# Kernel optimization log

Measured on AMD Instinct MI355X. Metric: run time of the kernel, lower is better.

## Reference

```python
import jax, jax.numpy as jnp
import numpy as np

N_BLOCKS = 16
N_HEADS = 2
HEAD_DIM = 32
SCALE = HEAD_DIM ** (-0.5)


def setup_inputs() -> dict:
    key = jax.random.key(0)
    ks = jax.random.split(key, 5)
    b, s, d = 16, 4096, 1024
    nb, bd = N_BLOCKS, 1024 // N_BLOCKS  # block_dim = 64; emb per-block dim = 64
    w_std = 1.0 / np.sqrt(bd)
    inp = {
        'x': jax.random.normal(ks[0], (b, s, d), dtype=jnp.float32),
        'wq': jax.random.normal(ks[1], (nb, bd, bd), dtype=jnp.float32) * w_std,
        'bq': jnp.zeros((nb, bd), dtype=jnp.float32),
        'wk': jax.random.normal(ks[2], (nb, bd, bd), dtype=jnp.float32) * w_std,
        'bk': jnp.zeros((nb, bd), dtype=jnp.float32),
        'wv': jax.random.normal(ks[3], (nb, bd, bd), dtype=jnp.float32) * w_std,
        'bv': jnp.zeros((nb, bd), dtype=jnp.float32),
        'wf': jax.random.normal(ks[4], (nb, bd, bd), dtype=jnp.float32) * w_std,
        'bf': jnp.zeros((nb, bd), dtype=jnp.float32),
    }
    return inp


def _group_linear(x, w, b):
    # x: [B, S, G*I] -> per-block linear -> [B, S, G*O]
    B, S, _ = x.shape
    G, I, O = w.shape
    xg = x.reshape(B, S, G, I)
    y = jnp.einsum('bsgi,gio->bsgo', xg, w) + b
    return y.reshape(B, S, G * O)


def reference(x, wq, bq, wk, bk, wv, bv, wf, bf):
    B, S, D = x.shape
    nb, nh, hd = N_BLOCKS, N_HEADS, HEAD_DIM
    # grouped QKV projections -> [B, S, nb, nh, hd] -> heads before blocks
    q = _group_linear(x, wq, bq).reshape(B, S, nb, nh, hd).transpose(0, 1, 3, 2, 4) * SCALE
    k = _group_linear(x, wk, bk).reshape(B, S, nb, nh, hd).transpose(0, 1, 3, 2, 4)
    v = _group_linear(x, wv, bv).reshape(B, S, nb, nh, hd).transpose(0, 1, 3, 2, 4)
    # attention across blocks: score [B, S, nh, nb, nb]
    score = jnp.einsum('bshgd,bshfd->bshgf', q, k)
    score = jax.nn.softmax(score, axis=-1)
    out = jnp.einsum('bshgf,bshfd->bshgd', score, v)
    # back to [B, S, nb, nh, hd] then flatten
    out = out.transpose(0, 1, 3, 2, 4).reshape(B, S, nb * nh * hd)
    out = _group_linear(out, wf, bf)
    return out.reshape(B, S, D)
```

## Files before the change

### kernel.cpp

```cpp
#include <hip/hip_runtime.h>
#include <hip/hip_bf16.h>
#include <stdint.h>


typedef __attribute__((ext_vector_type(8))) short bf16x8;
typedef __attribute__((ext_vector_type(4))) float f32x4;

#define NTOK   65536
#define DM     1024
#define TT     16
#define QSCALE 0.17677669529663687f
#define LOG2E  1.4426950408889634f

static __device__ __forceinline__ unsigned short f2bf(float f) {
  unsigned int u = __float_as_uint(f);
  u += 0x7fffu + ((u >> 16) & 1u);
  return (unsigned short)(u >> 16);
}

static __device__ __forceinline__ unsigned int pk2(float a, float b) {
  return (unsigned int)f2bf(a) | ((unsigned int)f2bf(b) << 16);
}

static __device__ __forceinline__ bf16x8 pack8(float4 a, float4 b) {
  bf16x8 r;
  r[0] = (short)f2bf(a.x); r[1] = (short)f2bf(a.y);
  r[2] = (short)f2bf(a.z); r[3] = (short)f2bf(a.w);
  r[4] = (short)f2bf(b.x); r[5] = (short)f2bf(b.y);
  r[6] = (short)f2bf(b.z); r[7] = (short)f2bf(b.w);
  return r;
}

union FragCast { uint4 u4; bf16x8 v; uint2 u2[2]; unsigned int u[4]; };

__global__ void build_wfrag(const float* __restrict__ wq, const float* __restrict__ wk,
                            const float* __restrict__ wv, const float* __restrict__ wf,
                            uint4* __restrict__ wfrag) {
  int tid = blockIdx.x * 256 + threadIdx.x;
  if (tid >= 4 * 16 * 2 * 4 * 64) return;
  int lane =  tid        & 63;
  int nf   = (tid >> 6)  & 3;
  int kk   = (tid >> 8)  & 1;
  int g    = (tid >> 9)  & 15;
  int mat  =  tid >> 13;
  const float* w = (mat == 0) ? wq : (mat == 1) ? wk : (mat == 2) ? wv : wf;
  float sc = (mat == 0) ? QSCALE : 1.0f;
  int o  = nf * 16 + (lane & 15);
  int kb = kk * 32 + 8 * (lane >> 4);
  unsigned int packed[4];
#pragma unroll
  for (int jj = 0; jj < 4; ++jj) {
    unsigned short lo = f2bf(w[(g * 64 + kb + 2 * jj    ) * 64 + o] * sc);
    unsigned short hi = f2bf(w[(g * 64 + kb + 2 * jj + 1) * 64 + o] * sc);
    packed[jj] = (unsigned int)lo | ((unsigned int)hi << 16);
  }
  uint4 u; u.x = packed[0]; u.y = packed[1]; u.z = packed[2]; u.w = packed[3];
  wfrag[tid] = u;
}

#define PH1(h_) do {                                                          \
  _Pragma("unroll")                                                           \
  for (int gi = 0; gi < 2; ++gi) {                                            \
    const int g = 2 * w + gi;                                                 \
    _Pragma("unroll")                                                         \
    for (int mat = 0; mat < 2; ++mat) {       \
      const float* bp = mat ? bk : bq;                                        \
      const float bsc = mat ? 1.0f : QSCALE;                                  \
      unsigned short* dst = mat ? s_k : s_q;                                  \
      _Pragma("unroll")                                                       \
      for (int nf2 = 0; nf2 < 2; ++nf2) {                                     \
        const int nf = 2 * (h_) + nf2;                                        \
        float4 b4 = *(const float4*)&bp[g * 64 + nf * 16 + 4 * lq];           \
        f32x4 a1 = {b4.x * bsc, b4.y * bsc, b4.z * bsc, b4.w * bsc};          \
        _Pragma("unroll")                                                     \
        for (int kk = 0; kk < 2; ++kk) {                                      \
          FragCast fc;                                                        \
          fc.u4 = wfrag[(((mat * 16 + g) * 2 + kk) * 4 + nf) * 64 + lane];    \
          a1 = __builtin_amdgcn_mfma_f32_16x16x32_bf16(fc.v, afr[gi][kk], a1, 0, 0, 0); \
        }                                                                     \
             \
        uint2 w2; w2.x = pk2(a1[0], a1[1]); w2.y = pk2(a1[2], a1[3]);         \
        const int blk = (16 * (2 * nf2 + (lq >> 1)) + g) ^ (lr & 7);          \
        *(uint2*)&dst[lr * 512 + blk * 8 + 4 * (lq & 1)] = w2;                \
      }                                                                       \
    }                                                                         \
    _Pragma("unroll")                                                         \
    for (int nf2 = 0; nf2 < 2; ++nf2) {         \
      const int nf = 2 * (h_) + nf2;                                          \
      const float bias = bv[g * 64 + nf * 16 + lr];                           \
      f32x4 a1 = {bias, bias, bias, bias};                                    \
      _Pragma("unroll")                                                       \
      for (int kk = 0; kk < 2; ++kk) {                                        \
        FragCast fc;                                                          \
        fc.u4 = wfrag[(((2 * 16 + g) * 2 + kk) * 4 + nf) * 64 + lane];        \
        a1 = __builtin_amdgcn_mfma_f32_16x16x32_bf16(afr[gi][kk], fc.v, a1, 0, 0, 0); \
      }                                                                       \
                   \
      const int L = 16 * (g >> 2) + lr;                                       \
      const int jj = g & 3;                                                   \
      _Pragma("unroll")                                                       \
      for (int r = 0; r < 4; ++r)                                             \
        s_v[((4 * lq + r) * 2 + nf2) * 256 + L * 4 + jj] = f2bf(a1[r]);       \
    }                                                                         \
  }                                                                           \
} while (0)

#define PH2() do {                                                            \
  _Pragma("unroll")                                                           \
  for (int tt = 0; tt < 2; ++tt) {                                            \
    const int t = 2 * w + tt;                                                 \
    f32x4 zero = {0.f, 0.f, 0.f, 0.f};                                        \
    FragCast qa, ka;                                                          \
    const int blk = lane ^ (t & 7);                                           \
    qa.u4 = *(const uint4*)&s_q[t * 512 + blk * 8];                           \
    ka.u4 = *(const uint4*)&s_k[t * 512 + blk * 8];                           \
                  \
    f32x4 sc4 = __builtin_amdgcn_mfma_f32_16x16x32_bf16(ka.v, qa.v, zero, 0, 0, 0); \
    float m = fmaxf(fmaxf(sc4[0], sc4[1]), fmaxf(sc4[2], sc4[3]));            \
    m = fmaxf(m, __shfl_xor(m, 16));                                          \
    m = fmaxf(m, __shfl_xor(m, 32));                                          \
    float p0 = exp2f((sc4[0] - m) * LOG2E);                                   \
    float p1 = exp2f((sc4[1] - m) * LOG2E);                                   \
    float p2 = exp2f((sc4[2] - m) * LOG2E);                                   \
    float p3 = exp2f((sc4[3] - m) * LOG2E);                                   \
    float s = p0 + p1 + p2 + p3;                                              \
    s += __shfl_xor(s, 16);                                                   \
    s += __shfl_xor(s, 32);                                                   \
    const float inv = __fdividef(1.0f, s);                                    \
    FragCast pa;                      \
    pa.u[0] = pk2(p0 * inv, p1 * inv);                                        \
    pa.u[1] = pk2(p2 * inv, p3 * inv);                                        \
    pa.u[2] = 0; pa.u[3] = 0;                                                 \
    _Pragma("unroll")                                                         \
    for (int nf = 0; nf < 2; ++nf) {                                          \
      FragCast va;              \
      va.u2[0] = *(const uint2*)&s_v[(t * 2 + nf) * 256 + lane * 4];          \
      va.u[2] = 0; va.u[3] = 0;                                               \
      f32x4 o4 = __builtin_amdgcn_mfma_f32_16x16x32_bf16(va.v, pa.v, zero, 0, 0, 0); \
                                   \
      uint2 w2; w2.x = pk2(o4[0], o4[1]); w2.y = pk2(o4[2], o4[3]);           \
      const int ablk = (16 * (2 * nf + (lq >> 1)) + lr) ^ (t & 7);            \
      *(uint2*)&s_att[t * 512 + ablk * 8 + 4 * (lq & 1)] = w2;                \
    }                                                                         \
  }                                                                           \
} while (0)

#define PH3(h_) do {                                                          \
  _Pragma("unroll")                                                           \
  for (int gi = 0; gi < 2; ++gi) {                                            \
    const int g = 2 * w + gi;                                                 \
    FragCast aa;                        \
    const int blk = (16 * lq + g) ^ (lr & 7);                                 \
    aa.u4 = *(const uint4*)&s_att[lr * 512 + blk * 8];                        \
    _Pragma("unroll")                                                         \
    for (int nf = 0; nf < 4; ++nf) {                                          \
      FragCast fc;                                                            \
      fc.u4 = wfrag[(((3 * 16 + g) * 2 + (h_)) * 4 + nf) * 64 + lane];        \
      acc[gi][nf] = __builtin_amdgcn_mfma_f32_16x16x32_bf16(fc.v, aa.v, acc[gi][nf], 0, 0, 0); \
    }                                                                         \
  }                                                                           \
} while (0)

__global__ __launch_bounds__(512, 4)
void fused_gc(const float* __restrict__ x,
              const float* __restrict__ bq, const float* __restrict__ bk,
              const float* __restrict__ bv, const float* __restrict__ bfb,
              const uint4* __restrict__ wfrag,
              float* __restrict__ out) {
  __shared__ __align__(16) unsigned short s_q  [16 * 512];
  __shared__ __align__(16) unsigned short s_k  [16 * 512];
  __shared__ __align__(16) unsigned short s_att[16 * 512];
  __shared__ __align__(16) unsigned short s_v  [16 * 2 * 64 * 4];

  const int tid  = threadIdx.x;
  const int w    = tid >> 6;
  const int lane = tid & 63;
  const int lr   = lane & 15;
  const int lq   = lane >> 4;
  const long tok0 = (long)blockIdx.x * TT;

  bf16x8 afr[2][2];
  {
    const float* xr = x + (tok0 + lr) * DM;
#pragma unroll
    for (int gi = 0; gi < 2; ++gi) {
      const int g = 2 * w + gi;
#pragma unroll
      for (int kk = 0; kk < 2; ++kk) {
        const float* p = xr + g * 64 + kk * 32 + 8 * lq;
        afr[gi][kk] = pack8(*(const float4*)p, *(const float4*)(p + 4));
      }
    }
  }

  f32x4 acc[2][4];

  PH1(0);
  __syncthreads();
  PH2();
  __syncthreads();

#pragma unroll
  for (int gi = 0; gi < 2; ++gi) {
    const int g = 2 * w + gi;
#pragma unroll
    for (int nf = 0; nf < 4; ++nf) {
      float4 b4 = *(const float4*)&bfb[g * 64 + nf * 16 + 4 * lq];
      acc[gi][nf][0] = b4.x; acc[gi][nf][1] = b4.y;
      acc[gi][nf][2] = b4.z; acc[gi][nf][3] = b4.w;
    }
  }
  PH3(0);
  PH1(1);
  __syncthreads();
  PH2();
  __syncthreads();
  PH3(1);

#pragma unroll
  for (int gi = 0; gi < 2; ++gi) {
    const int g = 2 * w + gi;
#pragma unroll
    for (int nf = 0; nf < 4; ++nf) {
      float4 o4;
      o4.x = acc[gi][nf][0]; o4.y = acc[gi][nf][1];
      o4.z = acc[gi][nf][2]; o4.w = acc[gi][nf][3];
      *(float4*)&out[(tok0 + lr) * DM + g * 64 + nf * 16 + 4 * lq] = o4;
    }
  }
}

extern "C" void kernel_launch(void* const* d_in, const int* in_sizes, int n_in,
                              void* d_out, int out_size, void* d_ws, size_t ws_size,
                              hipStream_t stream) {
  const float* x   = (const float*)d_in[0];
  const float* wq  = (const float*)d_in[1];
  const float* bq_ = (const float*)d_in[2];
  const float* wk  = (const float*)d_in[3];
  const float* bk_ = (const float*)d_in[4];
  const float* wv  = (const float*)d_in[5];
  const float* bv_ = (const float*)d_in[6];
  const float* wf  = (const float*)d_in[7];
  const float* bf_ = (const float*)d_in[8];
  (void)in_sizes; (void)n_in; (void)out_size; (void)ws_size;

  uint4* wfrag = (uint4*)d_ws;

  build_wfrag<<<128, 256, 0, stream>>>(wq, wk, wv, wf, wfrag);
  fused_gc<<<NTOK / TT, 512, 0, stream>>>(x, bq_, bk_, bv_, bf_, wfrag,
                                          (float*)d_out);
}
```

Measured before the change: 234.7 us.

## Make fused kernel loop over token tiles and prefetch next x tile

```diff
diff --git a/kernel.cpp b/kernel.cpp
--- a/kernel.cpp
+++ b/kernel.cpp
@@ -9,13 +9,14 @@
 #define NTOK   65536
 #define DM     1024
 #define TT     16
+#define NT     8
 #define QSCALE 0.17677669529663687f
 #define LOG2E  1.4426950408889634f
 
 static __device__ __forceinline__ unsigned short f2bf(float f) {
-  unsigned int u = __float_as_uint(f);
-  u += 0x7fffu + ((u >> 16) & 1u);
-  return (unsigned short)(u >> 16);
+  union { __hip_bfloat16 h; unsigned short s; } cv;
+  cv.h = __float2bfloat16(f);
+  return cv.s;
 }
 
 static __device__ __forceinline__ unsigned int pk2(float a, float b) {
@@ -161,72 +162,90 @@
   }                                                                           \
 } while (0)
 
+#define XLOAD(tokbase_) do {                                                  \
+  const float* xr = x + ((tokbase_) + lr) * DM + 2 * w * 64;                  \
+  xA0 = *(const float4*)(xr + 8 * lq);                                        \
+  xA1 = *(const float4*)(xr + 8 * lq + 4);                                    \
+  xA2 = *(const float4*)(xr + 32 + 8 * lq);                                   \
+  xA3 = *(const float4*)(xr + 32 + 8 * lq + 4);                               \
+  xB0 = *(const float4*)(xr + 64 + 8 * lq);                                   \
+  xB1 = *(const float4*)(xr + 64 + 8 * lq + 4);                               \
+  xB2 = *(const float4*)(xr + 96 + 8 * lq);                                   \
+  xB3 = *(const float4*)(xr + 96 + 8 * lq + 4);                               \
+} while (0)
+
+#define XPACK() do {                                                          \
+  afr[0][0] = pack8(xA0, xA1);                                                \
+  afr[0][1] = pack8(xA2, xA3);                                                \
+  afr[1][0] = pack8(xB0, xB1);                                                \
+  afr[1][1] = pack8(xB2, xB3);                                                \
+} while (0)
+
 __global__ __launch_bounds__(512, 4)
-void fused_gc(const float* __restrict__ x,
-              const float* __restrict__ bq, const float* __restrict__ bk,
-              const float* __restrict__ bv, const float* __restrict__ bfb,
-              const uint4* __restrict__ wfrag,
-              float* __restrict__ out) {
+void fused_pers16(const float* __restrict__ x,
+                  const float* __restrict__ bq, const float* __restrict__ bk,
+                  const float* __restrict__ bv, const float* __restrict__ bfb,
+                  const uint4* __restrict__ wfrag,
+                  float* __restrict__ out) {
   __shared__ __align__(16) unsigned short s_q  [16 * 512];
   __shared__ __align__(16) unsigned short s_k  [16 * 512];
   __shared__ __align__(16) unsigned short s_att[16 * 512];
-  __shared__ __align__(16) unsigned short s_v  [16 * 2 * 64 * 4];
+  __shared__ __align__(16) unsigned short s_v  [16 * 2 * 256];
 
   const int tid  = threadIdx.x;
   const int w    = tid >> 6;
   const int lane = tid & 63;
   const int lr   = lane & 15;
   const int lq   = lane >> 4;
-  const long tok0 = (long)blockIdx.x * TT;
 
   bf16x8 afr[2][2];
-  {
-    const float* xr = x + (tok0 + lr) * DM;
+  float4 xA0, xA1, xA2, xA3, xB0, xB1, xB2, xB3;
+  f32x4 acc[2][4];
+
+  const long base = (long)blockIdx.x * (NT * TT);
+  XLOAD(base);
+  XPACK();
+
+  for (int it = 0; it < NT; ++it) {
+    const long tok0 = base + (long)it * TT;
+
+    PH1(0);
+    __syncthreads();
+    PH2();
+    __syncthreads();
+
+    if (it + 1 < NT) XLOAD(tok0 + TT);
+
 #pragma unroll
     for (int gi = 0; gi < 2; ++gi) {
       const int g = 2 * w + gi;
 #pragma unroll
-      for (int kk = 0; kk < 2; ++kk) {
-        const float* p = xr + g * 64 + kk * 32 + 8 * lq;
-        afr[gi][kk] = pack8(*(const float4*)p, *(const float4*)(p + 4));
+      for (int nf = 0; nf < 4; ++nf) {
+        float4 b4 = *(const float4*)&bfb[g * 64 + nf * 16 + 4 * lq];
+        acc[gi][nf][0] = b4.x; acc[gi][nf][1] = b4.y;
+        acc[gi][nf][2] = b4.z; acc[gi][nf][3] = b4.w;
       }
     }
-  }
-
-  f32x4 acc[2][4];
-
-  PH1(0);
-  __syncthreads();
-  PH2();
-  __syncthreads();
-
-#pragma unroll
-  for (int gi = 0; gi < 2; ++gi) {
-    const int g = 2 * w + gi;
-#pragma unroll
-    for (int nf = 0; nf < 4; ++nf) {
-      float4 b4 = *(const float4*)&bfb[g * 64 + nf * 16 + 4 * lq];
-      acc[gi][nf][0] = b4.x; acc[gi][nf][1] = b4.y;
-      acc[gi][nf][2] = b4.z; acc[gi][nf][3] = b4.w;
+    PH3(0);
+    PH1(1);
+    __syncthreads();
+    PH2();
+    __syncthreads();
+    PH3(1);
+
+#pragma unroll
+    for (int gi = 0; gi < 2; ++gi) {
+      const int g = 2 * w + gi;
+#pragma unroll
+      for (int nf = 0; nf < 4; ++nf) {
+        float4 o4;
+        o4.x = acc[gi][nf][0]; o4.y = acc[gi][nf][1];
+        o4.z = acc[gi][nf][2]; o4.w = acc[gi][nf][3];
+        *(float4*)&out[(tok0 + lr) * DM + g * 64 + nf * 16 + 4 * lq] = o4;
+      }
     }
-  }
-  PH3(0);
-  PH1(1);
-  __syncthreads();
-  PH2();
-  __syncthreads();
-  PH3(1);
-
-#pragma unroll
-  for (int gi = 0; gi < 2; ++gi) {
-    const int g = 2 * w + gi;
-#pragma unroll
-    for (int nf = 0; nf < 4; ++nf) {
-      float4 o4;
-      o4.x = acc[gi][nf][0]; o4.y = acc[gi][nf][1];
-      o4.z = acc[gi][nf][2]; o4.w = acc[gi][nf][3];
-      *(float4*)&out[(tok0 + lr) * DM + g * 64 + nf * 16 + 4 * lq] = o4;
-    }
+
+    if (it + 1 < NT) XPACK();
   }
 }
 
@@ -247,6 +266,6 @@
   uint4* wfrag = (uint4*)d_ws;
 
   build_wfrag<<<128, 256, 0, stream>>>(wq, wk, wv, wf, wfrag);
-  fused_gc<<<NTOK / TT, 512, 0, stream>>>(x, bq_, bk_, bv_, bf_, wfrag,
-                                          (float*)d_out);
-}
+  fused_pers16<<<NTOK / (NT * TT), 512, 0, stream>>>(x, bq_, bk_, bv_, bf_,
+                                                     wfrag, (float*)d_out);
+}
```

Result: slower. 937.5 us (+299.4%).
